# Performance work log

Hardware: AMD Instinct MI355X
Metric: run time of the kernel (lower is better)

The kernel has to match this reference:

```python
import jax, jax.numpy as jnp
import numpy as np

B, T, IN, H, F = 512, 32, 8, 64, 1
IN1 = IN + F  # input_size + feats


def setup_inputs() -> dict:
    key = jax.random.key(0)
    ks = jax.random.split(key, 8)
    s = 0.05
    return {
        "input_data": jax.random.normal(ks[0], (B, T, IN), jnp.float32),
        "y_prev": jax.random.normal(ks[1], (B, T), jnp.float32),
        "Wv": jax.random.normal(ks[2], (H, H + IN1), jnp.float32) * s,
        "bv": jnp.zeros((H,), jnp.float32),
        "W_ih": jax.random.normal(ks[3], (4 * H, IN1), jnp.float32) * s,
        "W_hh": jax.random.normal(ks[4], (4 * H, H), jnp.float32) * s,
        "b_ih": jnp.zeros((4 * H,), jnp.float32),
        "b_hh": jnp.zeros((4 * H,), jnp.float32),
        "Wp": jax.random.normal(ks[5], (1, H + IN1), jnp.float32) * s,
        "bp": jnp.zeros((1,), jnp.float32),
        "Wf": jax.random.normal(ks[6], (F, H), jnp.float32) * s,
        "bf": jnp.zeros((F,), jnp.float32),
        "num_particles": 256,
    }


def _forward(input_data, y_prev, Wv, bv, W_ih, W_hh, b_ih, b_hh, Wp, bp, Wf, bf, num_particles):
    b, t_len, _ = input_data.shape
    h_dim = Wf.shape[1]
    P = num_particles
    noise_key = jax.random.key(1234)

    new_input = jnp.concatenate([input_data, y_prev[:, :, None]], axis=2)  # [B,T,IN1]
    xs = jnp.moveaxis(new_input, 1, 0)  # [T,B,IN1]
    h0 = jnp.zeros((P, b, h_dim), input_data.dtype)
    c0 = jnp.zeros((P, b, h_dim), input_data.dtype)

    def step(carry, xt_t):
        h, c = carry  # each [P,B,H], particle-major
        x_t, t = xt_t  # [B,IN1], scalar t
        hidden_mean = h.mean(axis=0)  # [B,H] (mean over particles)
        var = jnp.concatenate([x_t, hidden_mean], axis=1) @ Wv.T + bv  # [B,H]
        std = jax.nn.softplus(var)
        # single LSTM cell step over P*B "batch" rows (input tiled over particles)
        gates = x_t @ W_ih.T + b_ih + h @ W_hh.T + b_hh  # [P,B,4H]
        i, f, g, o = jnp.split(gates, 4, axis=-1)  # torch gate order i,f,g,o
        c_new = jax.nn.sigmoid(f) * c + jax.nn.sigmoid(i) * jnp.tanh(g)
        h_lstm = jax.nn.sigmoid(o) * jnp.tanh(c_new)
        # reparameterize: mu + eps*std (std broadcast over particle dim)
        eps = jax.random.normal(jax.random.fold_in(noise_key, t), (P, b, h_dim), h.dtype)
        h_rep = h_lstm + eps * std
        # sort_hidden: per batch element, reorder particles by fc_final projection
        proj = (h_rep @ Wf.T + bf)[..., 0]  # [P,B]
        order = jnp.argsort(proj, axis=0)  # [P,B]
        h_sorted = jnp.take_along_axis(h_rep, order[:, :, None], axis=0)
        y = jnp.concatenate([h_sorted, jnp.broadcast_to(x_t, (P, b, x_t.shape[1]))], axis=-1)
        logpdf = (y @ Wp.T + bp)[..., 0]  # [P,B]
        # faithful to torch's view(-1, P, 1) on a particle-major flat buffer
        pr = logpdf.reshape(-1).reshape(b, P)
        w_inc = jnp.exp(pr).mean(axis=1, keepdims=True)  # [B,1]
        return (h_sorted, c_new), w_inc

    (h_fin, _), w_incs = jax.lax.scan(step, (h0, c0), (xs, jnp.arange(t_len)))
    weights = w_incs.sum(axis=0)  # [B,1]
    y_pred = h_fin.mean(axis=0) @ Wf.T + bf  # [B,1]
    return y_pred, weights


def reference(input_data, y_prev, Wv, bv, W_ih, W_hh, b_ih, b_hh, Wp, bp, Wf, bf, num_particles):
    return _forward(input_data, y_prev, Wv, bv, W_ih, W_hh, b_ih, b_hh, Wp, bp, Wf, bf, num_particles)
```

## Files before the change

### kernel.cpp

```cpp
#include <hip/hip_runtime.h>
#include <stdint.h>

#define NB 512
#define NT 32
#define NIN 8
#define NIN1 9
#define NH 64
#define NP 256
#define NTHR 512
#define HROW 68

typedef __attribute__((ext_vector_type(8))) _Float16 f16x8;
typedef __attribute__((ext_vector_type(4))) float f32x4;

struct FKeys { uint32_t a[NT]; uint32_t b[NT]; };

__host__ __device__ __forceinline__ void tfr(uint32_t& x0, uint32_t& x1, int r) {
  x0 += x1; x1 = (x1 << r) | (x1 >> (32 - r)); x1 ^= x0;
}

__host__ __device__ __forceinline__ void threefry2x32(uint32_t k0, uint32_t k1,
                                                      uint32_t& x0, uint32_t& x1) {
  uint32_t k2 = k0 ^ k1 ^ 0x1BD11BDAu;
  x0 += k0; x1 += k1;
  tfr(x0,x1,13); tfr(x0,x1,15); tfr(x0,x1,26); tfr(x0,x1,6);
  x0 += k1; x1 += k2 + 1u;
  tfr(x0,x1,17); tfr(x0,x1,29); tfr(x0,x1,16); tfr(x0,x1,24);
  x0 += k2; x1 += k0 + 2u;
  tfr(x0,x1,13); tfr(x0,x1,15); tfr(x0,x1,26); tfr(x0,x1,6);
  x0 += k0; x1 += k1 + 3u;
  tfr(x0,x1,17); tfr(x0,x1,29); tfr(x0,x1,16); tfr(x0,x1,24);
  x0 += k1; x1 += k2 + 4u;
  tfr(x0,x1,13); tfr(x0,x1,15); tfr(x0,x1,26); tfr(x0,x1,6);
  x0 += k2; x1 += k0 + 5u;
}

__device__ __forceinline__ float normal_from_bits(uint32_t bits) {
  float f = __uint_as_float((bits >> 9) | 0x3f800000u) - 1.0f;
  const float lo = -0.99999994f;
  float u = fmaxf(lo, fmaf(f, 2.0f, lo));
  float w = -__logf(fmaf(-u, u, 1.0f));
  float p;
  if (w < 5.0f) {
    w -= 2.5f;
    p = 2.81022636e-08f;
    p = fmaf(p, w, 3.43273939e-07f);
    p = fmaf(p, w, -3.5233877e-06f);
    p = fmaf(p, w, -4.39150654e-06f);
    p = fmaf(p, w, 0.00021858087f);
    p = fmaf(p, w, -0.00125372503f);
    p = fmaf(p, w, -0.00417768164f);
    p = fmaf(p, w, 0.246640727f);
    p = fmaf(p, w, 1.50140941f);
  } else {
    w = sqrtf(w) - 3.0f;
    p = -0.000200214257f;
    p = fmaf(p, w, 0.000100950558f);
    p = fmaf(p, w, 0.00134934322f);
    p = fmaf(p, w, -0.00367342844f);
    p = fmaf(p, w, 0.00573950773f);
    p = fmaf(p, w, -0.0076224613f);
    p = fmaf(p, w, 0.00943887047f);
    p = fmaf(p, w, 1.00167406f);
    p = fmaf(p, w, 2.83297682f);
  }
  return 1.41421356f * (p * u);
}

__device__ __forceinline__ float frcp(float x) { return __builtin_amdgcn_rcpf(x); }
__device__ __forceinline__ float fsigmoid(float x) { return frcp(1.0f + __expf(-x)); }
__device__ __forceinline__ float ftanh(float x) { return 1.0f - 2.0f * frcp(1.0f + __expf(2.0f * x)); }

__device__ __forceinline__ uint32_t pack_f16(float x) {
  union { _Float16 h; uint16_t u; } c;
  c.h = (_Float16)x;
  return (uint32_t)c.u;
}
__device__ __forceinline__ _Float16 bits_to_h(uint16_t u) {
  union { _Float16 h; uint16_t u; } c;
  c.u = u;
  return c.h;
}

__device__ __forceinline__ f16x8 ld8h(const _Float16* p) {
  union { f16x8 v; uint64_t q[2]; } u;
  u.q[0] = *(const uint64_t*)(p);
  u.q[1] = *(const uint64_t*)(p + 4);
  return u.v;
}

__global__ __launch_bounds__(NTHR, 4)
void pf_main(const float* __restrict__ input_data, const float* __restrict__ y_prev,
             const float* __restrict__ Wv, const float* __restrict__ bv,
             const float* __restrict__ W_ih, const float* __restrict__ W_hh,
             const float* __restrict__ b_ih, const float* __restrict__ b_hh,
             const float* __restrict__ Wp, const float* __restrict__ bp,
             const float* __restrict__ Wf, const float* __restrict__ bf,
             float* __restrict__ out, float* __restrict__ gw,
             FKeys fk)
{
  __shared__ __align__(16) _Float16 h1_s[NP * HROW];
  __shared__ __align__(16) _Float16 c_s[16384];
  __shared__ __align__(16) float xg_s[NP];
  __shared__ __align__(16) float proj_s[NP];
  __shared__ float lp_s[NP];
  __shared__ float wsum_s[NP];
  __shared__ int   rankP_s[2 * NP];
  __shared__ float hsum_s[NH];
  __shared__ float std_s[NH];
  __shared__ float xs_s[16];

  const int tid  = threadIdx.x;
  const int b    = blockIdx.x;
  const int lane = tid & 63;
  const int wq   = tid >> 6;
  const int lrow = (lane >> 4) & 3;
  const int lcol = lane & 15;

  for (int i = tid; i < NP * HROW; i += NTHR) h1_s[i] = (_Float16)0.0f;
  for (int i = tid; i < 16384; i += NTHR) c_s[i] = (_Float16)0.0f;
  if (tid < NP) wsum_s[tid] = 0.0f;
  if (tid < NH) hsum_s[tid] = 0.0f;

  const float bf0 = bf[0];
  const float bp0 = bp[0];
  const uint32_t bsh = (uint32_t)b << 6;

  f16x8 w1f[2][2];
  #pragma unroll
  for (int kg2 = 0; kg2 < 2; ++kg2) {
    const int rpr  = 32 * wq + 16 * kg2 + lcol;
    const int orig = (rpr & 3) * NH + (rpr >> 2);
    #pragma unroll
    for (int kt = 0; kt < 2; ++kt) {
      #pragma unroll
      for (int e = 0; e < 8; ++e)
        w1f[kg2][kt][e] = (_Float16)W_hh[orig * NH + kt * 32 + lrow * 8 + e];
    }
  }

  float wf2[2], wp2[2];
  #pragma unroll
  for (int kg2 = 0; kg2 < 2; ++kg2) {
    const int k = 8 * wq + 4 * kg2 + lrow;
    wf2[kg2] = Wf[k];
    wp2[kg2] = Wp[k];
  }

  _Float16* cw = &c_s[wq * 2048 + lane];

  auto finalize_init = [&]() {
    if (tid < NH) {
      float v = bv[tid];
      const float* wvr = Wv + tid * (NIN1 + NH);
      #pragma unroll
      for (int i = 0; i < NIN1; ++i) v = fmaf(xs_s[i], wvr[i], v);
      #pragma unroll
      for (int k = 0; k < NH; ++k)
        v = fmaf(hsum_s[k] * (1.0f / NP), wvr[NIN1 + k], v);
      std_s[tid] = fmaxf(v, 0.0f) + log1pf(expf(-fabsf(v)));
    }
    if (tid < NP) {
      const int orow = (tid & 3) * NH + (tid >> 2);
      float a = b_ih[orow] + b_hh[orow];
      const float* wr = W_ih + orow * NIN1;
      #pragma unroll
      for (int i = 0; i < NIN1; ++i) a = fmaf(xs_s[i], wr[i], a);
      xg_s[tid] = a;
      proj_s[tid] = bf0;
      float xp = bp0;
      #pragma unroll
      for (int i = 0; i < NIN1; ++i) xp = fmaf(xs_s[i], Wp[NH + i], xp);
      lp_s[tid] = xp;
    }
  };

  if (tid < NIN) xs_s[tid] = input_data[(b * NT + 0) * NIN + tid];
  if (tid == NIN) xs_s[NIN] = y_prev[b * NT + 0];
  __syncthreads();
  finalize_init();
  __syncthreads();

  for (int t = 0; t < NT; ++t) {
    if (tid < 16 && t + 1 < NT) {
      if (tid < NIN) xs_s[tid] = input_data[(b * NT + t + 1) * NIN + tid];
      if (tid == NIN) xs_s[NIN] = y_prev[b * NT + t + 1];
    }

    float std2[2];
    #pragma unroll
    for (int kg2 = 0; kg2 < 2; ++kg2) std2[kg2] = std_s[8 * wq + 4 * kg2 + lrow];

    const uint32_t fk0 = fk.a[t], fk1 = fk.b[t];
    float hs2[2] = {0.0f, 0.0f};
    uint32_t shp[2][8];

    #pragma unroll
    for (int pt8 = 0; pt8 < 8; ++pt8) {
      const int p = 16 * pt8 + lcol;
      const f16x8 bA0 = ld8h(&h1_s[p * HROW + lrow * 8]);
      const f16x8 bA1 = ld8h(&h1_s[p * HROW + 32 + lrow * 8]);
      const f16x8 bB0 = ld8h(&h1_s[(p + 128) * HROW + lrow * 8]);
      const f16x8 bB1 = ld8h(&h1_s[(p + 128) * HROW + 32 + lrow * 8]);

      float plp = 0.0f, lpp = 0.0f, plp1 = 0.0f, lpp1 = 0.0f;
      #pragma unroll
      for (int kg2 = 0; kg2 < 2; ++kg2) {
        const int k = 8 * wq + 4 * kg2 + lrow;
        _Float16* cptr = cw + (kg2 * 8 + pt8) * 128;
        const float cvA = (float)cptr[0];
        const float cvB = (float)cptr[64];
        const float4 xgv = *(const float4*)&xg_s[32 * wq + 16 * kg2 + 4 * lrow];
        f32x4 accA, accB;
        accA[0] = xgv.x; accA[1] = xgv.y; accA[2] = xgv.z; accA[3] = xgv.w;
        accB = accA;
        accA = __builtin_amdgcn_mfma_f32_16x16x32_f16(w1f[kg2][0], bA0, accA, 0, 0, 0);
        accB = __builtin_amdgcn_mfma_f32_16x16x32_f16(w1f[kg2][0], bB0, accB, 0, 0, 0);
        accA = __builtin_amdgcn_mfma_f32_16x16x32_f16(w1f[kg2][1], bA1, accA, 0, 0, 0);
        accB = __builtin_amdgcn_mfma_f32_16x16x32_f16(w1f[kg2][1], bB1, accB, 0, 0, 0);
        float si = fsigmoid(accA[0]);
        float sf = fsigmoid(accA[1]);
        float so = fsigmoid(accA[3]);
        float cn = sf * cvA + si * ftanh(accA[2]);
        cptr[0] = (_Float16)cn;
        float hlA = so * ftanh(cn);
        float si2 = fsigmoid(accB[0]);
        float sf2 = fsigmoid(accB[1]);
        float so2 = fsigmoid(accB[3]);
        float cn2 = sf2 * cvB + si2 * ftanh(accB[2]);
        cptr[64] = (_Float16)cn2;
        float hlB = so2 * ftanh(cn2);
        uint32_t x0 = ((uint32_t)p << 15) | bsh | (uint32_t)k;
        uint32_t x1 = x0 + (1u << 22);
        threefry2x32(fk0, fk1, x0, x1);
        float hA = fmaf(normal_from_bits(x0), std2[kg2], hlA);
        float hB = fmaf(normal_from_bits(x1), std2[kg2], hlB);
        hs2[kg2] += hA + hB;
        plp  = fmaf(hA, wf2[kg2], plp);  lpp  = fmaf(hA, wp2[kg2], lpp);
        plp1 = fmaf(hB, wf2[kg2], plp1); lpp1 = fmaf(hB, wp2[kg2], lpp1);
        shp[kg2][pt8] = pack_f16(hA) | (pack_f16(hB) << 16);
      }
      plp  += __shfl_xor(plp, 16, 64);  plp  += __shfl_xor(plp, 32, 64);
      lpp  += __shfl_xor(lpp, 16, 64);  lpp  += __shfl_xor(lpp, 32, 64);
      plp1 += __shfl_xor(plp1, 16, 64); plp1 += __shfl_xor(plp1, 32, 64);
      lpp1 += __shfl_xor(lpp1, 16, 64); lpp1 += __shfl_xor(lpp1, 32, 64);
      if (lane < 16) {
        atomicAdd(&proj_s[p], plp);
        atomicAdd(&lp_s[p], lpp);
        atomicAdd(&proj_s[p + 128], plp1);
        atomicAdd(&lp_s[p + 128], lpp1);
      }
    }
    #pragma unroll
    for (int kg2 = 0; kg2 < 2; ++kg2) {
      float s = hs2[kg2];
      s += __shfl_xor(s, 1, 64); s += __shfl_xor(s, 2, 64);
      s += __shfl_xor(s, 4, 64); s += __shfl_xor(s, 8, 64);
      if (lcol == 0) hsum_s[8 * wq + 4 * kg2 + lrow] = s;
    }
    __syncthreads();

    {
      const int ph = tid & (NP - 1);
      const int hh = tid >> 8;
      const float pv = proj_s[ph];
      int rk = 0;
      const float4* c4 = (const float4*)proj_s;
      #pragma unroll 8
      for (int q4 = 32 * hh; q4 < 32 * hh + 32; ++q4) {
        float4 v = c4[q4];
        int qb = q4 * 4;
        rk += (v.x < pv || (v.x == pv && qb + 0 < ph)) ? 1 : 0;
        rk += (v.y < pv || (v.y == pv && qb + 1 < ph)) ? 1 : 0;
        rk += (v.z < pv || (v.z == pv && qb + 2 < ph)) ? 1 : 0;
        rk += (v.w < pv || (v.w == pv && qb + 3 < ph)) ? 1 : 0;
      }
      rankP_s[hh * NP + ph] = rk;
    }
    __syncthreads();

    if (tid < NP) {
      const int rank = rankP_s[tid] + rankP_s[NP + tid];
      wsum_s[rank] += __expf(lp_s[tid]);
    }
    #pragma unroll
    for (int kg2 = 0; kg2 < 2; ++kg2) {
      const int k = 8 * wq + 4 * kg2 + lrow;
      #pragma unroll
      for (int pt8 = 0; pt8 < 8; ++pt8) {
        const int p = 16 * pt8 + lcol;
        const int rA = rankP_s[p] + rankP_s[NP + p];
        const int rB = rankP_s[p + 128] + rankP_s[NP + p + 128];
        const uint32_t v = shp[kg2][pt8];
        h1_s[rA * HROW + k] = bits_to_h((uint16_t)(v & 0xffffu));
        h1_s[rB * HROW + k] = bits_to_h((uint16_t)(v >> 16));
      }
    }
    finalize_init();
    __syncthreads();
  }

  if (tid < NH) {
    float hm = hsum_s[tid] * (1.0f / NP);
    float contrib = hm * Wf[tid];
    contrib += __shfl_xor(contrib, 32, 64);
    contrib += __shfl_xor(contrib, 16, 64);
    contrib += __shfl_xor(contrib, 8, 64);
    contrib += __shfl_xor(contrib, 4, 64);
    contrib += __shfl_xor(contrib, 2, 64);
    contrib += __shfl_xor(contrib, 1, 64);
    if (tid == 0) out[b] = contrib + bf0;
  }
  if (tid < NP) gw[(size_t)tid * NB + b] = wsum_s[tid];
}

__global__ __launch_bounds__(64, 1)
void pf_weights(const float* __restrict__ gw, float* __restrict__ out) {
  int i = blockIdx.x;
  int lane = threadIdx.x;
  const float* src = gw + ((size_t)(i >> 1)) * NB + (size_t)(i & 1) * NP;
  float4 v = ((const float4*)src)[lane];
  float s = (v.x + v.y) + (v.z + v.w);
  s += __shfl_xor(s, 32, 64);
  s += __shfl_xor(s, 16, 64);
  s += __shfl_xor(s, 8, 64);
  s += __shfl_xor(s, 4, 64);
  s += __shfl_xor(s, 2, 64);
  s += __shfl_xor(s, 1, 64);
  if (lane == 0) out[NB + i] = s * (1.0f / NP);
}

extern "C" void kernel_launch(void* const* d_in, const int* in_sizes, int n_in,
                              void* d_out, int out_size, void* d_ws, size_t ws_size,
                              hipStream_t stream) {
  (void)in_sizes; (void)n_in; (void)out_size; (void)ws_size;
  const float* input_data = (const float*)d_in[0];
  const float* y_prev     = (const float*)d_in[1];
  const float* Wv         = (const float*)d_in[2];
  const float* bv         = (const float*)d_in[3];
  const float* W_ih       = (const float*)d_in[4];
  const float* W_hh       = (const float*)d_in[5];
  const float* b_ih       = (const float*)d_in[6];
  const float* b_hh       = (const float*)d_in[7];
  const float* Wp         = (const float*)d_in[8];
  const float* bp         = (const float*)d_in[9];
  const float* Wf         = (const float*)d_in[10];
  const float* bf         = (const float*)d_in[11];
  float* out = (float*)d_out;
  float* gw  = (float*)d_ws;

  FKeys fk;
  for (int t = 0; t < NT; ++t) {
    uint32_t x0 = 0u, x1 = (uint32_t)t;
    threefry2x32(0u, 1234u, x0, x1);
    fk.a[t] = x0; fk.b[t] = x1;
  }

  pf_main<<<dim3(NB), dim3(NTHR), 0, stream>>>(
      input_data, y_prev, Wv, bv, W_ih, W_hh, b_ih, b_hh, Wp, bp, Wf, bf,
      out, gw, fk);
  pf_weights<<<dim3(NB), dim3(64), 0, stream>>>(gw, out);
}
```

Before: 1.131 ms.

## Precompute Gaussian noise in a separate kernel and stream it into the main loop

Adds a pf_eps kernel that generates all threefry-derived normal samples as packed fp16 pairs in workspace memory. The main kernel then loads them per timestep instead of running threefry plus Box-Muller inline. This takes the RNG ALU work off the latency-bound recurrent kernel and spreads it across a fully parallel prologue. In exchange it writes and reads about 512 MB of noise through HBM, rounds the noise to fp16, and needs a large workspace, falling back to inline generation if the workspace is too small.

```diff
diff --git a/kernel.cpp b/kernel.cpp
--- a/kernel.cpp
+++ b/kernel.cpp
@@ -81,6 +81,12 @@
   c.u = u;
   return c.h;
 }
+__device__ __forceinline__ float f16_lo(uint32_t w) {
+  union { _Float16 h; uint16_t u; } c; c.u = (uint16_t)(w & 0xffffu); return (float)c.h;
+}
+__device__ __forceinline__ float f16_hi(uint32_t w) {
+  union { _Float16 h; uint16_t u; } c; c.u = (uint16_t)(w >> 16); return (float)c.h;
+}
 
 __device__ __forceinline__ f16x8 ld8h(const _Float16* p) {
   union { f16x8 v; uint64_t q[2]; } u;
@@ -89,6 +95,20 @@
   return u.v;
 }
 
+__global__ __launch_bounds__(256)
+void pf_eps(uint32_t* __restrict__ eps, FKeys fk) {
+  const uint32_t g  = blockIdx.x * 256u + threadIdx.x;
+  const uint32_t pp = g & 127u;
+  const uint32_t k  = (g >> 7) & 63u;
+  const uint32_t t  = (g >> 13) & 31u;
+  const uint32_t b  = g >> 18;
+  uint32_t x0 = (pp << 15) | (b << 6) | k;
+  uint32_t x1 = x0 + (1u << 22);
+  threefry2x32(fk.a[t], fk.b[t], x0, x1);
+  eps[g] = pack_f16(normal_from_bits(x0)) | (pack_f16(normal_from_bits(x1)) << 16);
+}
+
+template <bool USE_EPS>
 __global__ __launch_bounds__(NTHR, 4)
 void pf_main(const float* __restrict__ input_data, const float* __restrict__ y_prev,
              const float* __restrict__ Wv, const float* __restrict__ bv,
@@ -97,7 +117,7 @@
              const float* __restrict__ Wp, const float* __restrict__ bp,
              const float* __restrict__ Wf, const float* __restrict__ bf,
              float* __restrict__ out, float* __restrict__ gw,
-             FKeys fk)
+             const uint32_t* __restrict__ eps, FKeys fk)
 {
   __shared__ __align__(16) _Float16 h1_s[NP * HROW];
   __shared__ __align__(16) _Float16 c_s[16384];
@@ -194,6 +214,18 @@
     const uint32_t fk0 = fk.a[t], fk1 = fk.b[t];
     float hs2[2] = {0.0f, 0.0f};
     uint32_t shp[2][8];
+
+    uint32_t epsr[16];
+    if constexpr (USE_EPS) {
+      const uint32_t* epst = eps + ((size_t)(b * NT + t) << 13);
+      #pragma unroll
+      for (int kg2 = 0; kg2 < 2; ++kg2) {
+        const int k = 8 * wq + 4 * kg2 + lrow;
+        #pragma unroll
+        for (int pt8 = 0; pt8 < 8; ++pt8)
+          epsr[kg2 * 8 + pt8] = epst[k * 128 + 16 * pt8 + lcol];
+      }
+    }
 
     #pragma unroll
     for (int pt8 = 0; pt8 < 8; ++pt8) {
@@ -230,11 +262,20 @@
         float cn2 = sf2 * cvB + si2 * ftanh(accB[2]);
         cptr[64] = (_Float16)cn2;
         float hlB = so2 * ftanh(cn2);
-        uint32_t x0 = ((uint32_t)p << 15) | bsh | (uint32_t)k;
-        uint32_t x1 = x0 + (1u << 22);
-        threefry2x32(fk0, fk1, x0, x1);
-        float hA = fmaf(normal_from_bits(x0), std2[kg2], hlA);
-        float hB = fmaf(normal_from_bits(x1), std2[kg2], hlB);
+        float eA, eB;
+        if constexpr (USE_EPS) {
+          const uint32_t ev = epsr[kg2 * 8 + pt8];
+          eA = f16_lo(ev);
+          eB = f16_hi(ev);
+        } else {
+          uint32_t x0 = ((uint32_t)p << 15) | bsh | (uint32_t)k;
+          uint32_t x1 = x0 + (1u << 22);
+          threefry2x32(fk0, fk1, x0, x1);
+          eA = normal_from_bits(x0);
+          eB = normal_from_bits(x1);
+        }
+        float hA = fmaf(eA, std2[kg2], hlA);
+        float hB = fmaf(eB, std2[kg2], hlB);
         hs2[kg2] += hA + hB;
         plp  = fmaf(hA, wf2[kg2], plp);  lpp  = fmaf(hA, wp2[kg2], lpp);
         plp1 = fmaf(hB, wf2[kg2], plp1); lpp1 = fmaf(hB, wp2[kg2], lpp1);
@@ -333,7 +374,7 @@
 extern "C" void kernel_launch(void* const* d_in, const int* in_sizes, int n_in,
                               void* d_out, int out_size, void* d_ws, size_t ws_size,
                               hipStream_t stream) {
-  (void)in_sizes; (void)n_in; (void)out_size; (void)ws_size;
+  (void)in_sizes; (void)n_in; (void)out_size;
   const float* input_data = (const float*)d_in[0];
   const float* y_prev     = (const float*)d_in[1];
   const float* Wv         = (const float*)d_in[2];
@@ -356,8 +397,20 @@
     fk.a[t] = x0; fk.b[t] = x1;
   }
 
-  pf_main<<<dim3(NB), dim3(NTHR), 0, stream>>>(
-      input_data, y_prev, Wv, bv, W_ih, W_hh, b_ih, b_hh, Wp, bp, Wf, bf,
-      out, gw, fk);
+  const size_t gw_bytes  = (size_t)NP * NB * sizeof(float);
+  const size_t eps_elems = (size_t)NB * NT * NH * 128;
+  const size_t need      = gw_bytes + eps_elems * sizeof(uint32_t);
+
+  if (ws_size >= need) {
+    uint32_t* eps = (uint32_t*)(gw + (size_t)NP * NB);
+    pf_eps<<<dim3((unsigned)(eps_elems / 256)), dim3(256), 0, stream>>>(eps, fk);
+    pf_main<true><<<dim3(NB), dim3(NTHR), 0, stream>>>(
+        input_data, y_prev, Wv, bv, W_ih, W_hh, b_ih, b_hh, Wp, bp, Wf, bf,
+        out, gw, eps, fk);
+  } else {
+    pf_main<false><<<dim3(NB), dim3(NTHR), 0, stream>>>(
+        input_data, y_prev, Wv, bv, W_ih, W_hh, b_ih, b_hh, Wp, bp, Wf, bf,
+        out, gw, nullptr, fk);
+  }
   pf_weights<<<dim3(NB), dim3(64), 0, stream>>>(gw, out);
 }
```

Result: no change. 1.128 ms (-0.3%).
